# Performance work log

Measured on AMD Instinct MI355X. Metric: run time of the kernel, lower is better.

Reference implementation:

```python
import jax, jax.numpy as jnp
import numpy as np

EPS = 1e-6
H = 8          # num_heads
GAMMA = 0.99   # fixed decay (requires_grad=False in source)
RPE_LAYERS = 3


def srms(x):
    # SimpleRMSNorm: x / (rms(x) + eps), rms = ||x||_2 / sqrt(d) = sqrt(mean(x^2))
    return x / (jnp.sqrt(jnp.mean(x * x, axis=-1, keepdims=True)) + EPS)


def setup_inputs() -> dict:
    key = jax.random.key(0)
    B, N, E = 8, 2048, 512
    D1 = 1536            # int(3*512) // 8 * 8
    R = 512              # rpe_embedding
    ks = jax.random.split(key, 12)

    def lin(k, i, o):
        return jax.random.normal(k, (i, o), jnp.float32) * (i ** -0.5)

    x = jax.random.normal(ks[0], (B, N, E), jnp.float32)
    return {
        "x": x,
        "Wu": lin(ks[1], E, D1), "bu": jnp.zeros((D1,), jnp.float32),
        "Wv": lin(ks[2], E, D1), "bv": jnp.zeros((D1,), jnp.float32),
        "Wo": lin(ks[3], D1, E), "bo": jnp.zeros((E,), jnp.float32),
        "rpe_Win": lin(ks[4], 1, R), "rpe_bin": jnp.zeros((R,), jnp.float32),
        "rpe_W": jax.random.normal(ks[5], (RPE_LAYERS, R, R), jnp.float32) * (R ** -0.5),
        "rpe_b": jnp.zeros((RPE_LAYERS, R), jnp.float32),
        "rpe_Wout": lin(ks[6], R, D1), "rpe_bout": jnp.zeros((D1,), jnp.float32),
    }


def reference(x, Wu, bu, Wv, bv, Wo, bo, rpe_Win, rpe_bin, rpe_W, rpe_b, rpe_Wout, rpe_bout):
    B, N, E = x.shape
    u = jax.nn.silu(x @ Wu + bu)                     # b n d1
    v = jax.nn.silu(x @ Wv + bv)                     # b n d1
    D1 = v.shape[-1]
    D = D1 // H
    v = v.reshape(B, N, H, D).transpose(0, 2, 1, 3)  # b h n d

    # RPE MLP over positions: row 0 is the zero index, rows 1..N-1 are pos indices 1..N-1 (par_type=1)
    idx = jnp.arange(0, N, dtype=x.dtype)[:, None]   # (N, 1)
    h = idx @ rpe_Win + rpe_bin                      # (N, R)
    for i in range(RPE_LAYERS):                      # residual=False
        h = jax.nn.relu(srms(h)) @ rpe_W[i] + rpe_b[i]
    coeffs = jax.nn.relu(srms(h)) @ rpe_Wout + rpe_bout   # (N, H*D)
    coeffs = coeffs.reshape(N, H, D).transpose(1, 0, 2)   # h n d

    zero = coeffs[:, :1]                             # h 1 d  (a_0)
    pos = coeffs[:, 1:]                              # h n-1 d (a_1..a_{n-1})
    decay = GAMMA ** jnp.arange(1, N, dtype=x.dtype)[None, :, None]
    pos = pos * decay
    # causal: a = [a0, a1..a_{n-1}, a0]; act_type='none' -> identity
    a = jnp.concatenate([zero, pos, zero], axis=1)   # h, n+1, d

    # Toeplitz mixing via circular convolution of length 2n (torch.fft.rfft/irfft, norm='backward')
    m = 2 * N
    yf = jnp.fft.rfft(v, m, axis=2)                  # b h m/2+1 d (complex)
    af = jnp.fft.rfft(a, m, axis=1)[None]            # 1 h m/2+1 d
    out = jnp.fft.irfft(yf * af, m, axis=2)[:, :, :N, :]  # b h n d

    out = out.transpose(0, 2, 1, 3).reshape(B, N, D1)     # b n (h d)
    out = u * out
    return out @ Wo + bo
```

## Files before the change

### kernel.cpp

```cpp
#include <hip/hip_runtime.h>
#include <cstdint>


typedef unsigned short ushort_t;
typedef __attribute__((ext_vector_type(8))) short short8;
typedef __attribute__((ext_vector_type(4))) float f32x4;

#define AS1 __attribute__((address_space(1)))
#define AS3 __attribute__((address_space(3)))

__device__ __forceinline__ float bf2f(ushort_t b) {
  union { unsigned u; float f; } x; x.u = ((unsigned)b) << 16; return x.f;
}
__device__ __forceinline__ ushort_t f2bf(float f) {
  union { float f; unsigned u; } x; x.f = f;
  unsigned r = x.u + 0x7fffu + ((x.u >> 16) & 1u);
  return (ushort_t)(r >> 16);
}

__device__ __forceinline__ void gload_lds16(const void* g, void* l) {
  auto gp = reinterpret_cast<const AS1 unsigned*>(reinterpret_cast<uintptr_t>(g));
  auto lp = reinterpret_cast<AS3 unsigned*>(reinterpret_cast<uintptr_t>(l));
  __builtin_amdgcn_global_load_lds(gp, lp, 16, 0, 0);
}

template<int MODE>
__launch_bounds__(256, 2)
__global__ void gemm_bt(const ushort_t* __restrict__ A, const ushort_t* __restrict__ Bt,
                        const float* __restrict__ bias, void* __restrict__ Cout,
                        void* __restrict__ Cout2, int M, int N, int K, float lng)
{
  __shared__ ushort_t As[128 * 64];
  __shared__ ushort_t Bs[128 * 64];
  const int tid  = threadIdx.x;
  const int wave = tid >> 6, lane = tid & 63;
  const int nb = N >> 7;
  const int bm = (int)blockIdx.x / nb, bn = (int)blockIdx.x % nb;
  const int m0 = bm << 7, n0 = bn << 7;
  const int lrow = lane & 15, quad = lane >> 4;
  const int wm = (wave >> 1) << 6, wn = (wave & 1) << 6;
  const int srow = lane >> 3;
  const int scol = (lane & 7) << 3;

  f32x4 acc[4][4] = {};

  for (int kt = 0; kt < K; kt += 64) {
    __syncthreads();
#pragma unroll
    for (int i = 0; i < 4; ++i) {
      const int ci  = i * 4 + wave;
      const int row = ci * 8 + srow;
      gload_lds16(A  + (long)(m0 + row) * K + kt + scol, (void*)&As[ci * 512]);
      gload_lds16(Bt + (long)(n0 + row) * K + kt + scol, (void*)&Bs[ci * 512]);
    }
    __syncthreads();
#pragma unroll
    for (int s = 0; s < 2; ++s) {
      short8 afr[4], bfr[4];
#pragma unroll
      for (int i = 0; i < 4; ++i)
        afr[i] = *(const short8*)&As[(wm + i * 16 + lrow) * 64 + s * 32 + quad * 8];
#pragma unroll
      for (int j = 0; j < 4; ++j)
        bfr[j] = *(const short8*)&Bs[(wn + j * 16 + lrow) * 64 + s * 32 + quad * 8];
#pragma unroll
      for (int i = 0; i < 4; ++i)
#pragma unroll
        for (int j = 0; j < 4; ++j)
          acc[i][j] = __builtin_amdgcn_mfma_f32_16x16x32_bf16(afr[i], bfr[j], acc[i][j], 0, 0, 0);
    }
  }

#pragma unroll
  for (int i = 0; i < 4; ++i) {
    const int rowb = m0 + wm + i * 16 + quad * 4;
#pragma unroll
    for (int j = 0; j < 4; ++j) {
      const int col = n0 + wn + j * 16 + lrow;
      const float bv = bias[col];
      if (MODE == 0) {
#pragma unroll
        for (int r = 0; r < 4; ++r)
          ((float*)Cout)[(long)(rowb + r) * N + col] = acc[i][j][r] + bv;
      } else if (MODE == 2) {
#pragma unroll
        for (int r = 0; r < 4; ++r) {
          const int row = rowb + r;
          float dec = __expf(lng * (float)row);
          ((float*)Cout)[(long)col * M + row] = (acc[i][j][r] + bv) * dec;
        }
      } else {
        if (col < 1536) {
#pragma unroll
          for (int r = 0; r < 4; ++r) {
            float val = acc[i][j][r] + bv;
            float sv = val / (1.f + __expf(-val));
            ((ushort_t*)Cout)[(long)(rowb + r) * 1536 + col] = f2bf(sv);
          }
        } else {
          union { ushort_t h[4]; uint2 u2; } pk;
#pragma unroll
          for (int r = 0; r < 4; ++r) {
            float val = acc[i][j][r] + bv;
            float sv = val / (1.f + __expf(-val));
            pk.h[r] = f2bf(sv);
          }
          *(uint2*)((ushort_t*)Cout2 + (long)(col - 1536) * 16384 + rowb) = pk.u2;
        }
      }
    }
  }
}

__launch_bounds__(256)
__global__ void wtrans(const float* __restrict__ src, ushort_t* __restrict__ dst, int K, int N)
{
  __shared__ float tile[32][33];
  const int nbx = N >> 5;
  const int bx = (int)blockIdx.x % nbx, by = (int)blockIdx.x / nbx;
  const int n0 = bx << 5, k0 = by << 5;
  const int tx = threadIdx.x & 31, ty = threadIdx.x >> 5;
  for (int yy = ty; yy < 32; yy += 8)
    tile[yy][tx] = src[(long)(k0 + yy) * N + n0 + tx];
  __syncthreads();
  for (int yy = ty; yy < 32; yy += 8)
    dst[(long)(n0 + yy) * K + k0 + tx] = f2bf(tile[tx][yy]);
}

__launch_bounds__(256)
__global__ void concat_bias(const float* __restrict__ a, const float* __restrict__ b,
                            float* __restrict__ dst)
{
  int i = blockIdx.x * 256 + threadIdx.x;
  if (i < 1536) { dst[i] = a[i]; dst[1536 + i] = b[i]; }
}

__launch_bounds__(256)
__global__ void cvt_bf16(const float* __restrict__ src, ushort_t* __restrict__ dst)
{
  long i = (long)(blockIdx.x * 256 + threadIdx.x) * 4;
  float4 f = *(const float4*)(src + i);
  unsigned lo = (unsigned)f2bf(f.x) | ((unsigned)f2bf(f.y) << 16);
  unsigned hi = (unsigned)f2bf(f.z) | ((unsigned)f2bf(f.w) << 16);
  *(uint2*)(dst + i) = make_uint2(lo, hi);
}

__device__ __forceinline__ void srms_relu_store(float v0, float v1, ushort_t* out,
                                                long rowbase, int tid)
{
  float ss = v0 * v0 + v1 * v1;
#pragma unroll
  for (int off = 32; off; off >>= 1) ss += __shfl_down(ss, off);
  __shared__ float ps[4];
  const int wave = tid >> 6, lane = tid & 63;
  if (lane == 0) ps[wave] = ss;
  __syncthreads();
  float tot = ps[0] + ps[1] + ps[2] + ps[3];
  float sc = 1.f / (sqrtf(tot * (1.f / 512.f)) + 1e-6f);
  out[rowbase + tid]       = f2bf(fmaxf(v0 * sc, 0.f));
  out[rowbase + tid + 256] = f2bf(fmaxf(v1 * sc, 0.f));
}

__launch_bounds__(256)
__global__ void rpe_h0(const float* __restrict__ Win, const float* __restrict__ bin,
                       ushort_t* __restrict__ out)
{
  const int n = blockIdx.x, tid = threadIdx.x;
  const float fn = (float)n;
  float v0 = fn * Win[tid] + bin[tid];
  float v1 = fn * Win[tid + 256] + bin[tid + 256];
  srms_relu_store(v0, v1, out, (long)n * 512, tid);
}

__launch_bounds__(256)
__global__ void rpe_norm(const float* __restrict__ h, ushort_t* __restrict__ out)
{
  const int n = blockIdx.x, tid = threadIdx.x;
  float v0 = h[(long)n * 512 + tid];
  float v1 = h[(long)n * 512 + tid + 256];
  srms_relu_store(v0, v1, out, (long)n * 512, tid);
}

__device__ __forceinline__ float2 cmulf(float2 a, float2 b) {
  return make_float2(a.x * b.x - a.y * b.y, a.x * b.y + a.y * b.x);
}

__device__ void fft2048_lds(float2* bx, float2* by, const float2* tw, int tid)
{
  for (int i = tid; i < 1024; i += 256) {
    float2 a = bx[i], b = bx[i + 1024];
    by[2 * i]     = make_float2(a.x + b.x, a.y + b.y);
    by[2 * i + 1] = make_float2(a.x - b.x, a.y - b.y);
  }
  __syncthreads();
  float2* src = by; float2* dst = bx;
  for (int ps = 0; ps < 5; ++ps) {
    const int p = 2 << (2 * ps);
    const int ts = 512 / p;
    for (int i = tid; i < 512; i += 256) {
      const int k = i & (p - 1);
      float2 u0 = src[i], u1 = src[i + 512], u2 = src[i + 1024], u3 = src[i + 1536];
      const int tb = k * ts;
      float2 w1 = tw[tb], w2 = tw[2 * tb], w3 = tw[3 * tb];
      u1 = cmulf(u1, w1); u2 = cmulf(u2, w2); u3 = cmulf(u3, w3);
      float2 v0 = make_float2(u0.x + u2.x, u0.y + u2.y);
      float2 v2 = make_float2(u0.x - u2.x, u0.y - u2.y);
      float2 v1 = make_float2(u1.x + u3.x, u1.y + u3.y);
      float2 v3 = make_float2(u1.y - u3.y, u3.x - u1.x);
      const int j = ((i - k) << 2) + k;
      dst[j]         = make_float2(v0.x + v1.x, v0.y + v1.y);
      dst[j + p]     = make_float2(v2.x + v3.x, v2.y + v3.y);
      dst[j + 2 * p] = make_float2(v0.x - v1.x, v0.y - v1.y);
      dst[j + 3 * p] = make_float2(v2.x - v3.x, v2.y - v3.y);
    }
    __syncthreads();
    float2* t = src; src = dst; dst = t;
  }
}

__device__ __forceinline__ void build_tw(float2* tw, int tid)
{
  for (int j = tid; j < 2048; j += 256) {
    float s, c; __sincosf((float)j * (6.283185307179586f / 2048.f), &s, &c);
    tw[j] = make_float2(c, -s);
  }
}

__launch_bounds__(256)
__global__ void fft_kernel_spec(const float* __restrict__ kern, float2* __restrict__ af)
{
  __shared__ float2 bx[2048], by[2048], tw[2048];
  const int tid = threadIdx.x, c = blockIdx.x;
  build_tw(tw, tid);
  const float* kc = kern + (long)c * 2048;
  for (int j = tid; j < 1024; j += 256) bx[j] = *(const float2*)(kc + 2 * j);
  for (int j = tid + 1024; j < 2048; j += 256) bx[j] = make_float2(0.f, 0.f);
  __syncthreads();
  fft2048_lds(bx, by, tw, tid);
  float2* afc = af + (long)c * 2052;
  for (int k = tid; k <= 1024; k += 256) {
    float2 Zk = bx[k], Zn = bx[(2048 - k) & 2047];
    float2 E = make_float2(0.5f * (Zk.x + Zn.x), 0.5f * (Zk.y - Zn.y));
    float2 O = make_float2(0.5f * (Zk.y + Zn.y), 0.5f * (Zn.x - Zk.x));
    float s, co; __sincosf((float)k * (3.14159265358979f / 2048.f), &s, &co);
    float2 W = make_float2(co, -s);
    float2 WO = cmulf(W, O);
    afc[k] = make_float2(E.x + WO.x, E.y + WO.y);
    if (k != 0 && k != 1024)
      afc[2048 - k] = make_float2(E.x - WO.x, -(E.y - WO.y));
    if (k == 0)
      afc[2048] = make_float2(E.x - WO.x, -(E.y - WO.y));
  }
}

__launch_bounds__(256)
__global__ void fft_conv(ushort_t* __restrict__ vt, const float2* __restrict__ af)
{
  __shared__ float2 bx[2048], by[2048], tw[2048];
  const int tid = threadIdx.x;
  const int c = (int)blockIdx.x >> 3;
  build_tw(tw, tid);
  ushort_t* vs = vt + (long)blockIdx.x * 2048;
  for (int j = tid; j < 1024; j += 256) {
    unsigned pv = *(const unsigned*)(vs + 2 * j);
    bx[j] = make_float2(bf2f((ushort_t)(pv & 0xffffu)), bf2f((ushort_t)(pv >> 16)));
  }
  for (int j = tid + 1024; j < 2048; j += 256) bx[j] = make_float2(0.f, 0.f);
  __syncthreads();
  fft2048_lds(bx, by, tw, tid);
  const float2* afc = af + (long)c * 2052;
  for (int k = tid; k <= 1024; k += 256) {
    float2 Zk = bx[k], Zn = bx[(2048 - k) & 2047];
    float2 E = make_float2(0.5f * (Zk.x + Zn.x), 0.5f * (Zk.y - Zn.y));
    float2 O = make_float2(0.5f * (Zk.y + Zn.y), 0.5f * (Zn.x - Zk.x));
    float s, co; __sincosf((float)k * (3.14159265358979f / 2048.f), &s, &co);
    float2 W = make_float2(co, -s);
    float2 WO = cmulf(W, O);
    float2 Xk = make_float2(E.x + WO.x, E.y + WO.y);
    float2 Xn = make_float2(E.x - WO.x, -(E.y - WO.y));
    float2 Pk = cmulf(Xk, afc[k]);
    float2 Pn = cmulf(Xn, afc[2048 - k]);
    float2 E2 = make_float2(0.5f * (Pk.x + Pn.x), 0.5f * (Pk.y - Pn.y));
    float2 G  = make_float2(0.5f * (Pk.x - Pn.x), 0.5f * (Pk.y + Pn.y));
    float2 cW = make_float2(W.x, -W.y);
    float2 Fo = cmulf(cW, G);
    by[k] = make_float2(E2.x - Fo.y, -(E2.y + Fo.x));
    if (k != 0 && k != 1024)
      by[2048 - k] = make_float2(E2.x + Fo.y, E2.y - Fo.x);
  }
  __syncthreads();
  fft2048_lds(by, bx, tw, tid);
  const float inv = 1.f / 2048.f;
  for (int j = tid; j < 1024; j += 256) {
    float2 r = by[j];
    unsigned ov = (unsigned)f2bf(r.x * inv) | ((unsigned)f2bf(-r.y * inv) << 16);
    *(unsigned*)(vs + 2 * j) = ov;
  }
}

__launch_bounds__(256)
__global__ void gate_trans(const ushort_t* __restrict__ convt, ushort_t* __restrict__ u)
{
  __shared__ ushort_t tile[64][65];
  const int bc = (int)blockIdx.x % 24, br = (int)blockIdx.x / 24;
  const int c0 = bc << 6, r0 = br << 6;
  const int tx = threadIdx.x & 63, ty = threadIdx.x >> 6;
  for (int yy = ty; yy < 64; yy += 4)
    tile[yy][tx] = convt[(long)(c0 + yy) * 16384 + r0 + tx];
  __syncthreads();
  for (int yy = ty; yy < 64; yy += 4) {
    long ui = (long)(r0 + yy) * 1536 + c0 + tx;
    float uu = bf2f(u[ui]);
    float cc = bf2f(tile[tx][yy]);
    u[ui] = f2bf(uu * cc);
  }
}

extern "C" void kernel_launch(void* const* d_in, const int* in_sizes, int n_in,
                              void* d_out, int out_size, void* d_ws, size_t ws_size,
                              hipStream_t stream)
{
  const float* x     = (const float*)d_in[0];
  const float* Wu    = (const float*)d_in[1];
  const float* bu    = (const float*)d_in[2];
  const float* Wv    = (const float*)d_in[3];
  const float* bv    = (const float*)d_in[4];
  const float* Wo    = (const float*)d_in[5];
  const float* bo    = (const float*)d_in[6];
  const float* rWin  = (const float*)d_in[7];
  const float* rbin  = (const float*)d_in[8];
  const float* rW    = (const float*)d_in[9];
  const float* rb    = (const float*)d_in[10];
  const float* rWout = (const float*)d_in[11];
  const float* rbout = (const float*)d_in[12];

  char* base = (char*)d_ws;
  size_t off = 0;
  auto alloc = [&](size_t bytes) -> char* {
    size_t r = (off + 255) & ~(size_t)255; off = r + bytes; return base + r;
  };
  ushort_t* wuvt   = (ushort_t*)alloc(3072L * 512 * 2);
  ushort_t* wot    = (ushort_t*)alloc(512L * 1536 * 2);
  ushort_t* wrt    = (ushort_t*)alloc(3L * 512 * 512 * 2);
  ushort_t* wroutt = (ushort_t*)alloc(1536L * 512 * 2);
  float*    buvb   = (float*)   alloc(3072L * 4);
  ushort_t* a0     = (ushort_t*)alloc(2048L * 512 * 2);
  float2*   af     = (float2*)  alloc(1536L * 2052 * 8);
  char*     X      = alloc(16384L * 512 * 2);
  ushort_t* u      = (ushort_t*)alloc(16384L * 1536 * 2);
  ushort_t* vt     = (ushort_t*)alloc(1536L * 16384 * 2);
  ushort_t* xb   = (ushort_t*)X;
  float*    h    = (float*)X;
  float*    kern = (float*)(X + 4L * 1024 * 1024);

  const float lng = -0.01005033585350145f;

  wtrans<<<dim3(768), dim3(256), 0, stream>>>(Wu, wuvt, 512, 1536);
  wtrans<<<dim3(768), dim3(256), 0, stream>>>(Wv, wuvt + 1536L * 512, 512, 1536);
  wtrans<<<dim3(768), dim3(256), 0, stream>>>(Wo, wot, 1536, 512);
  for (int i = 0; i < 3; ++i)
    wtrans<<<dim3(256), dim3(256), 0, stream>>>(rW + (long)i * 512 * 512,
                                                wrt + (long)i * 512 * 512, 512, 512);
  wtrans<<<dim3(768), dim3(256), 0, stream>>>(rWout, wroutt, 512, 1536);
  concat_bias<<<dim3(6), dim3(256), 0, stream>>>(bu, bv, buvb);
  cvt_bf16<<<dim3(8192), dim3(256), 0, stream>>>(x, xb);

  gemm_bt<3><<<dim3(3072), dim3(256), 0, stream>>>(xb, wuvt, buvb, u, vt,
                                                   16384, 3072, 512, 0.f);

  rpe_h0<<<dim3(2048), dim3(256), 0, stream>>>(rWin, rbin, a0);
  for (int i = 0; i < 3; ++i) {
    gemm_bt<0><<<dim3(64), dim3(256), 0, stream>>>(a0, wrt + (long)i * 512 * 512,
                                                   rb + (long)i * 512, h, nullptr,
                                                   2048, 512, 512, 0.f);
    rpe_norm<<<dim3(2048), dim3(256), 0, stream>>>(h, a0);
  }
  gemm_bt<2><<<dim3(192), dim3(256), 0, stream>>>(a0, wroutt, rbout, kern, nullptr,
                                                  2048, 1536, 512, lng);
  fft_kernel_spec<<<dim3(1536), dim3(256), 0, stream>>>(kern, af);

  fft_conv<<<dim3(12288), dim3(256), 0, stream>>>(vt, af);
  gate_trans<<<dim3(6144), dim3(256), 0, stream>>>(vt, u);
  gemm_bt<0><<<dim3(512), dim3(256), 0, stream>>>(u, wot, bo, d_out, nullptr,
                                                  16384, 512, 1536, 0.f);
}
```

Baseline: 560.0 us.

## Fuse prep kernels, precompute FFT twiddles globally, and swizzle FFT LDS accesses

Merges weight transposes, bias concat, input bf16 conversion, twiddle generation and the first RPE layer into one prep kernel to cut launch count. FFT kernels now read precomputed twiddle tables from global memory instead of computing sincos per block, which drops a 16KB LDS table and raises possible occupancy. LDS indices in the radix-4 FFT are XOR-swizzled to reduce bank conflicts, and the inner loops are fully unrolled. Twiddles now come from global/cache reads, which adds some memory traffic.

```diff
diff --git a/kernel.cpp b/kernel.cpp
--- a/kernel.cpp
+++ b/kernel.cpp
@@ -8,6 +8,8 @@
 
 #define AS1 __attribute__((address_space(1)))
 #define AS3 __attribute__((address_space(3)))
+
+#define SWZ(j) ((j) ^ (((j) >> 4) & 14))
 
 __device__ __forceinline__ float bf2f(ushort_t b) {
   union { unsigned u; float f; } x; x.u = ((unsigned)b) << 16; return x.f;
@@ -112,39 +114,6 @@
   }
 }
 
-__launch_bounds__(256)
-__global__ void wtrans(const float* __restrict__ src, ushort_t* __restrict__ dst, int K, int N)
-{
-  __shared__ float tile[32][33];
-  const int nbx = N >> 5;
-  const int bx = (int)blockIdx.x % nbx, by = (int)blockIdx.x / nbx;
-  const int n0 = bx << 5, k0 = by << 5;
-  const int tx = threadIdx.x & 31, ty = threadIdx.x >> 5;
-  for (int yy = ty; yy < 32; yy += 8)
-    tile[yy][tx] = src[(long)(k0 + yy) * N + n0 + tx];
-  __syncthreads();
-  for (int yy = ty; yy < 32; yy += 8)
-    dst[(long)(n0 + yy) * K + k0 + tx] = f2bf(tile[tx][yy]);
-}
-
-__launch_bounds__(256)
-__global__ void concat_bias(const float* __restrict__ a, const float* __restrict__ b,
-                            float* __restrict__ dst)
-{
-  int i = blockIdx.x * 256 + threadIdx.x;
-  if (i < 1536) { dst[i] = a[i]; dst[1536 + i] = b[i]; }
-}
-
-__launch_bounds__(256)
-__global__ void cvt_bf16(const float* __restrict__ src, ushort_t* __restrict__ dst)
-{
-  long i = (long)(blockIdx.x * 256 + threadIdx.x) * 4;
-  float4 f = *(const float4*)(src + i);
-  unsigned lo = (unsigned)f2bf(f.x) | ((unsigned)f2bf(f.y) << 16);
-  unsigned hi = (unsigned)f2bf(f.z) | ((unsigned)f2bf(f.w) << 16);
-  *(uint2*)(dst + i) = make_uint2(lo, hi);
-}
-
 __device__ __forceinline__ void srms_relu_store(float v0, float v1, ushort_t* out,
                                                 long rowbase, int tid)
 {
@@ -162,17 +131,6 @@
 }
 
 __launch_bounds__(256)
-__global__ void rpe_h0(const float* __restrict__ Win, const float* __restrict__ bin,
-                       ushort_t* __restrict__ out)
-{
-  const int n = blockIdx.x, tid = threadIdx.x;
-  const float fn = (float)n;
-  float v0 = fn * Win[tid] + bin[tid];
-  float v1 = fn * Win[tid + 256] + bin[tid + 256];
-  srms_relu_store(v0, v1, out, (long)n * 512, tid);
-}
-
-__launch_bounds__(256)
 __global__ void rpe_norm(const float* __restrict__ h, ushort_t* __restrict__ out)
 {
   const int n = blockIdx.x, tid = threadIdx.x;
@@ -181,25 +139,101 @@
   srms_relu_store(v0, v1, out, (long)n * 512, tid);
 }
 
+__device__ __forceinline__ void wtrans_body(const float* __restrict__ src,
+                                            ushort_t* __restrict__ dst,
+                                            int K, int N, int lb, int tid,
+                                            float (*tile)[33])
+{
+  const int nbx = N >> 5;
+  const int bx = lb % nbx, by = lb / nbx;
+  const int n0 = bx << 5, k0 = by << 5;
+  const int tx = tid & 31, ty = tid >> 5;
+  for (int yy = ty; yy < 32; yy += 8)
+    tile[yy][tx] = src[(long)(k0 + yy) * N + n0 + tx];
+  __syncthreads();
+  for (int yy = ty; yy < 32; yy += 8)
+    dst[(long)(n0 + yy) * K + k0 + tx] = f2bf(tile[tx][yy]);
+}
+
+__launch_bounds__(256)
+__global__ void prep_all(const float* __restrict__ Wu, const float* __restrict__ Wv,
+                         const float* __restrict__ Wo, const float* __restrict__ rW,
+                         const float* __restrict__ rWout,
+                         const float* __restrict__ bu, const float* __restrict__ bv,
+                         const float* __restrict__ x,
+                         const float* __restrict__ rWin, const float* __restrict__ rbin,
+                         ushort_t* __restrict__ wuvt, ushort_t* __restrict__ wot,
+                         ushort_t* __restrict__ wrt, ushort_t* __restrict__ wroutt,
+                         float* __restrict__ buvb, ushort_t* __restrict__ xb,
+                         float2* __restrict__ twg, float2* __restrict__ twh,
+                         ushort_t* __restrict__ a0)
+{
+  __shared__ float tile[32][33];
+  const int bid = blockIdx.x, tid = threadIdx.x;
+  if (bid < 3840) {
+    const float* src; ushort_t* dst; int K, N, lb;
+    if (bid < 768)       { src = Wu;    dst = wuvt;              K = 512;  N = 1536; lb = bid; }
+    else if (bid < 1536) { src = Wv;    dst = wuvt + 1536L*512;  K = 512;  N = 1536; lb = bid - 768; }
+    else if (bid < 2304) { src = Wo;    dst = wot;               K = 1536; N = 512;  lb = bid - 1536; }
+    else if (bid < 2560) { src = rW;              dst = wrt;              K = 512; N = 512; lb = bid - 2304; }
+    else if (bid < 2816) { src = rW + 512L*512;   dst = wrt + 512L*512;   K = 512; N = 512; lb = bid - 2560; }
+    else if (bid < 3072) { src = rW + 2L*512*512; dst = wrt + 2L*512*512; K = 512; N = 512; lb = bid - 2816; }
+    else                 { src = rWout; dst = wroutt;            K = 512;  N = 1536; lb = bid - 3072; }
+    wtrans_body(src, dst, K, N, lb, tid, tile);
+  } else if (bid < 3846) {
+    int i = (bid - 3840) * 256 + tid;
+    if (i < 1536) { buvb[i] = bu[i]; buvb[1536 + i] = bv[i]; }
+  } else if (bid < 12038) {
+    long i = (long)(bid - 3846) * 1024 + tid * 4;
+    float4 f = *(const float4*)(x + i);
+    unsigned lo = (unsigned)f2bf(f.x) | ((unsigned)f2bf(f.y) << 16);
+    unsigned hi = (unsigned)f2bf(f.z) | ((unsigned)f2bf(f.w) << 16);
+    *(uint2*)(xb + i) = make_uint2(lo, hi);
+  } else if (bid < 12046) {
+    int j = (bid - 12038) * 256 + tid;
+    float s, c;
+    __sincosf((float)j * (6.283185307179586f / 2048.f), &s, &c);
+    twg[j] = make_float2(c, -s);
+    if (j <= 1024) {
+      float s2, c2;
+      __sincosf((float)j * (3.14159265358979f / 2048.f), &s2, &c2);
+      twh[j] = make_float2(c2, -s2);
+    }
+  } else {
+    const int n = bid - 12046;
+    const float fn = (float)n;
+    float v0 = fn * rWin[tid] + rbin[tid];
+    float v1 = fn * rWin[tid + 256] + rbin[tid + 256];
+    srms_relu_store(v0, v1, a0, (long)n * 512, tid);
+  }
+}
+
 __device__ __forceinline__ float2 cmulf(float2 a, float2 b) {
   return make_float2(a.x * b.x - a.y * b.y, a.x * b.y + a.y * b.x);
 }
 
-__device__ void fft2048_lds(float2* bx, float2* by, const float2* tw, int tid)
-{
-  for (int i = tid; i < 1024; i += 256) {
-    float2 a = bx[i], b = bx[i + 1024];
-    by[2 * i]     = make_float2(a.x + b.x, a.y + b.y);
-    by[2 * i + 1] = make_float2(a.x - b.x, a.y - b.y);
+__device__ void fft2048_lds(float2* bx, float2* by, const float2* __restrict__ tw, int tid)
+{
+#pragma unroll
+  for (int ii = 0; ii < 4; ++ii) {
+    const int i = tid + ii * 256;
+    float2 a = bx[SWZ(i)], b = bx[SWZ(i + 1024)];
+    const int s = SWZ(2 * i);
+    by[s]     = make_float2(a.x + b.x, a.y + b.y);
+    by[s + 1] = make_float2(a.x - b.x, a.y - b.y);
   }
   __syncthreads();
   float2* src = by; float2* dst = bx;
+#pragma unroll
   for (int ps = 0; ps < 5; ++ps) {
     const int p = 2 << (2 * ps);
     const int ts = 512 / p;
-    for (int i = tid; i < 512; i += 256) {
+#pragma unroll
+    for (int ii = 0; ii < 2; ++ii) {
+      const int i = tid + ii * 256;
       const int k = i & (p - 1);
-      float2 u0 = src[i], u1 = src[i + 512], u2 = src[i + 1024], u3 = src[i + 1536];
+      float2 u0 = src[SWZ(i)],        u1 = src[SWZ(i + 512)];
+      float2 u2 = src[SWZ(i + 1024)], u3 = src[SWZ(i + 1536)];
       const int tb = k * ts;
       float2 w1 = tw[tb], w2 = tw[2 * tb], w3 = tw[3 * tb];
       u1 = cmulf(u1, w1); u2 = cmulf(u2, w2); u3 = cmulf(u3, w3);
@@ -208,42 +242,33 @@
       float2 v1 = make_float2(u1.x + u3.x, u1.y + u3.y);
       float2 v3 = make_float2(u1.y - u3.y, u3.x - u1.x);
       const int j = ((i - k) << 2) + k;
-      dst[j]         = make_float2(v0.x + v1.x, v0.y + v1.y);
-      dst[j + p]     = make_float2(v2.x + v3.x, v2.y + v3.y);
-      dst[j + 2 * p] = make_float2(v0.x - v1.x, v0.y - v1.y);
-      dst[j + 3 * p] = make_float2(v2.x - v3.x, v2.y - v3.y);
+      dst[SWZ(j)]         = make_float2(v0.x + v1.x, v0.y + v1.y);
+      dst[SWZ(j + p)]     = make_float2(v2.x + v3.x, v2.y + v3.y);
+      dst[SWZ(j + 2*p)]   = make_float2(v0.x - v1.x, v0.y - v1.y);
+      dst[SWZ(j + 3*p)]   = make_float2(v2.x - v3.x, v2.y - v3.y);
     }
     __syncthreads();
     float2* t = src; src = dst; dst = t;
   }
 }
 
-__device__ __forceinline__ void build_tw(float2* tw, int tid)
-{
-  for (int j = tid; j < 2048; j += 256) {
-    float s, c; __sincosf((float)j * (6.283185307179586f / 2048.f), &s, &c);
-    tw[j] = make_float2(c, -s);
-  }
-}
-
 __launch_bounds__(256)
-__global__ void fft_kernel_spec(const float* __restrict__ kern, float2* __restrict__ af)
-{
-  __shared__ float2 bx[2048], by[2048], tw[2048];
+__global__ void fft_kernel_spec(const float* __restrict__ kern, float2* __restrict__ af,
+                                const float2* __restrict__ twg, const float2* __restrict__ twh)
+{
+  __shared__ float2 bx[2048], by[2048];
   const int tid = threadIdx.x, c = blockIdx.x;
-  build_tw(tw, tid);
   const float* kc = kern + (long)c * 2048;
-  for (int j = tid; j < 1024; j += 256) bx[j] = *(const float2*)(kc + 2 * j);
-  for (int j = tid + 1024; j < 2048; j += 256) bx[j] = make_float2(0.f, 0.f);
-  __syncthreads();
-  fft2048_lds(bx, by, tw, tid);
+  for (int j = tid; j < 1024; j += 256) bx[SWZ(j)] = *(const float2*)(kc + 2 * j);
+  for (int j = tid + 1024; j < 2048; j += 256) bx[SWZ(j)] = make_float2(0.f, 0.f);
+  __syncthreads();
+  fft2048_lds(bx, by, twg, tid);
   float2* afc = af + (long)c * 2052;
   for (int k = tid; k <= 1024; k += 256) {
-    float2 Zk = bx[k], Zn = bx[(2048 - k) & 2047];
+    float2 Zk = bx[SWZ(k)], Zn = bx[SWZ((2048 - k) & 2047)];
     float2 E = make_float2(0.5f * (Zk.x + Zn.x), 0.5f * (Zk.y - Zn.y));
     float2 O = make_float2(0.5f * (Zk.y + Zn.y), 0.5f * (Zn.x - Zk.x));
-    float s, co; __sincosf((float)k * (3.14159265358979f / 2048.f), &s, &co);
-    float2 W = make_float2(co, -s);
+    float2 W = twh[k];
     float2 WO = cmulf(W, O);
     afc[k] = make_float2(E.x + WO.x, E.y + WO.y);
     if (k != 0 && k != 1024)
@@ -254,27 +279,26 @@
 }
 
 __launch_bounds__(256)
-__global__ void fft_conv(ushort_t* __restrict__ vt, const float2* __restrict__ af)
-{
-  __shared__ float2 bx[2048], by[2048], tw[2048];
+__global__ void fft_conv(ushort_t* __restrict__ vt, const float2* __restrict__ af,
+                         const float2* __restrict__ twg, const float2* __restrict__ twh)
+{
+  __shared__ float2 bx[2048], by[2048];
   const int tid = threadIdx.x;
   const int c = (int)blockIdx.x >> 3;
-  build_tw(tw, tid);
   ushort_t* vs = vt + (long)blockIdx.x * 2048;
   for (int j = tid; j < 1024; j += 256) {
     unsigned pv = *(const unsigned*)(vs + 2 * j);
-    bx[j] = make_float2(bf2f((ushort_t)(pv & 0xffffu)), bf2f((ushort_t)(pv >> 16)));
-  }
-  for (int j = tid + 1024; j < 2048; j += 256) bx[j] = make_float2(0.f, 0.f);
-  __syncthreads();
-  fft2048_lds(bx, by, tw, tid);
+    bx[SWZ(j)] = make_float2(bf2f((ushort_t)(pv & 0xffffu)), bf2f((ushort_t)(pv >> 16)));
+  }
+  for (int j = tid + 1024; j < 2048; j += 256) bx[SWZ(j)] = make_float2(0.f, 0.f);
+  __syncthreads();
+  fft2048_lds(bx, by, twg, tid);
   const float2* afc = af + (long)c * 2052;
   for (int k = tid; k <= 1024; k += 256) {
-    float2 Zk = bx[k], Zn = bx[(2048 - k) & 2047];
+    float2 Zk = bx[SWZ(k)], Zn = bx[SWZ((2048 - k) & 2047)];
     float2 E = make_float2(0.5f * (Zk.x + Zn.x), 0.5f * (Zk.y - Zn.y));
     float2 O = make_float2(0.5f * (Zk.y + Zn.y), 0.5f * (Zn.x - Zk.x));
-    float s, co; __sincosf((float)k * (3.14159265358979f / 2048.f), &s, &co);
-    float2 W = make_float2(co, -s);
+    float2 W = twh[k];
     float2 WO = cmulf(W, O);
     float2 Xk = make_float2(E.x + WO.x, E.y + WO.y);
     float2 Xn = make_float2(E.x - WO.x, -(E.y - WO.y));
@@ -284,15 +308,17 @@
     float2 G  = make_float2(0.5f * (Pk.x - Pn.x), 0.5f * (Pk.y + Pn.y));
     float2 cW = make_float2(W.x, -W.y);
     float2 Fo = cmulf(cW, G);
-    by[k] = make_float2(E2.x - Fo.y, -(E2.y + Fo.x));
-    if (k != 0 && k != 1024)
-      by[2048 - k] = make_float2(E2.x + Fo.y, E2.y - Fo.x);
-  }
-  __syncthreads();
-  fft2048_lds(by, bx, tw, tid);
+    by[SWZ(k)] = make_float2(E2.x - Fo.y, -(E2.y + Fo.x));
+    if (k != 0 && k != 1024) {
+      const int kn = 2048 - k;
+      by[SWZ(kn)] = make_float2(E2.x + Fo.y, E2.y - Fo.x);
+    }
+  }
+  __syncthreads();
+  fft2048_lds(by, bx, twg, tid);
   const float inv = 1.f / 2048.f;
   for (int j = tid; j < 1024; j += 256) {
-    float2 r = by[j];
+    float2 r = by[SWZ(j)];
     unsigned ov = (unsigned)f2bf(r.x * inv) | ((unsigned)f2bf(-r.y * inv) << 16);
     *(unsigned*)(vs + 2 * j) = ov;
   }
@@ -346,6 +372,8 @@
   float*    buvb   = (float*)   alloc(3072L * 4);
   ushort_t* a0     = (ushort_t*)alloc(2048L * 512 * 2);
   float2*   af     = (float2*)  alloc(1536L * 2052 * 8);
+  float2*   twg    = (float2*)  alloc(2048L * 8);
+  float2*   twh    = (float2*)  alloc(1025L * 8);
   char*     X      = alloc(16384L * 512 * 2);
   ushort_t* u      = (ushort_t*)alloc(16384L * 1536 * 2);
   ushort_t* vt     = (ushort_t*)alloc(1536L * 16384 * 2);
@@ -355,20 +383,13 @@
 
   const float lng = -0.01005033585350145f;
 
-  wtrans<<<dim3(768), dim3(256), 0, stream>>>(Wu, wuvt, 512, 1536);
-  wtrans<<<dim3(768), dim3(256), 0, stream>>>(Wv, wuvt + 1536L * 512, 512, 1536);
-  wtrans<<<dim3(768), dim3(256), 0, stream>>>(Wo, wot, 1536, 512);
-  for (int i = 0; i < 3; ++i)
-    wtrans<<<dim3(256), dim3(256), 0, stream>>>(rW + (long)i * 512 * 512,
-                                                wrt + (long)i * 512 * 512, 512, 512);
-  wtrans<<<dim3(768), dim3(256), 0, stream>>>(rWout, wroutt, 512, 1536);
-  concat_bias<<<dim3(6), dim3(256), 0, stream>>>(bu, bv, buvb);
-  cvt_bf16<<<dim3(8192), dim3(256), 0, stream>>>(x, xb);
+  prep_all<<<dim3(14094), dim3(256), 0, stream>>>(
+      Wu, Wv, Wo, rW, rWout, bu, bv, x, rWin, rbin,
+      wuvt, wot, wrt, wroutt, buvb, xb, twg, twh, a0);
 
   gemm_bt<3><<<dim3(3072), dim3(256), 0, stream>>>(xb, wuvt, buvb, u, vt,
                                                    16384, 3072, 512, 0.f);
 
-  rpe_h0<<<dim3(2048), dim3(256), 0, stream>>>(rWin, rbin, a0);
   for (int i = 0; i < 3; ++i) {
     gemm_bt<0><<<dim3(64), dim3(256), 0, stream>>>(a0, wrt + (long)i * 512 * 512,
                                                    rb + (long)i * 512, h, nullptr,
@@ -377,9 +398,9 @@
   }
   gemm_bt<2><<<dim3(192), dim3(256), 0, stream>>>(a0, wroutt, rbout, kern, nullptr,
                                                   2048, 1536, 512, lng);
-  fft_kernel_spec<<<dim3(1536), dim3(256), 0, stream>>>(kern, af);
-
-  fft_conv<<<dim3(12288), dim3(256), 0, stream>>>(vt, af);
+  fft_kernel_spec<<<dim3(1536), dim3(256), 0, stream>>>(kern, af, twg, twh);
+
+  fft_conv<<<dim3(12288), dim3(256), 0, stream>>>(vt, af, twg, twh);
   gate_trans<<<dim3(6144), dim3(256), 0, stream>>>(vt, u);
   gemm_bt<0><<<dim3(512), dim3(256), 0, stream>>>(u, wot, bo, d_out, nullptr,
                                                   16384, 512, 1536, 0.f);
```

New measurement: 530.8 us. 5.2% less time.
